# Performance work log

Measured on AMD Instinct MI355X. Metric: run time of the kernel, lower is better.

Reference implementation:

```python
import jax, jax.numpy as jnp
import numpy as np

N_NODES = 100000
N_EDGES = 600000
N_ETYPES = 3
N_LAYERS = 3  # n_layers + 1 conv layers
D = 128
EPS = 1e-5


def setup_inputs() -> dict:
    key = jax.random.key(0)
    ks = jax.random.split(key, 8)
    scale = 1.0 / np.sqrt(D)
    x = jax.random.normal(ks[0], (N_NODES, D), dtype=jnp.float32)
    src = jax.random.randint(ks[1], (N_ETYPES, N_EDGES), 0, N_NODES, dtype=jnp.int32)
    dst = jax.random.randint(ks[2], (N_ETYPES, N_EDGES), 0, N_NODES, dtype=jnp.int32)
    W_self = jax.random.normal(ks[3], (N_LAYERS, N_ETYPES, D, D), dtype=jnp.float32) * scale
    W_neigh = jax.random.normal(ks[4], (N_LAYERS, N_ETYPES, D, D), dtype=jnp.float32) * scale
    b = jax.random.normal(ks[5], (N_LAYERS, N_ETYPES, D), dtype=jnp.float32) * 0.01
    gamma = jnp.ones((N_LAYERS, D), dtype=jnp.float32)
    beta = jnp.zeros((N_LAYERS, D), dtype=jnp.float32)
    return {"x": x, "src": src, "dst": dst, "W_self": W_self, "W_neigh": W_neigh,
            "b": b, "gamma": gamma, "beta": beta}


def reference(x, src, dst, W_self, W_neigh, b, gamma, beta):
    N = x.shape[0]
    L, K = W_self.shape[0], W_self.shape[1]
    # in-degree per etype (DGL mean aggregator: zero-degree -> 0 neighbor feat)
    degs = [jnp.clip(jax.ops.segment_sum(jnp.ones((dst.shape[1],), x.dtype), dst[k],
                                         num_segments=N), 1.0, None)
            for k in range(K)]
    h = x
    for l in range(L):
        acc = jnp.zeros((N, W_self.shape[-1]), x.dtype)
        for k in range(K):
            # gather src feats, mean-aggregate onto dst: [N, D]
            neigh = jax.ops.segment_sum(h[src[k]], dst[k], num_segments=N) / degs[k][:, None]
            o = h @ W_self[l, k] + neigh @ W_neigh[l, k] + b[l, k]
            if l < L - 1:  # activation inside SAGEConv, last layer has none
                o = jax.nn.relu(o)
            acc = acc + o  # HeteroGraphConv aggregate='sum'
        # BatchNorm1d, training mode (biased batch variance)
        mu = acc.mean(axis=0)
        var = ((acc - mu) ** 2).mean(axis=0)
        h = gamma[l] * (acc - mu) / jnp.sqrt(var + EPS) + beta[l]
    return h
```

## Files before the change

kernel.cpp:

```cpp
#include <hip/hip_runtime.h>

#define NN 100000
#define NNP 100096
#define NE 600000
#define KE 3
#define NL 3
#define D  128
#define EPS 1e-5f
#define NB 391
#define NBKT 196
#define EPB 4096
#define NEB 147
#define NSL 16

typedef __attribute__((ext_vector_type(8))) short short8;
typedef __attribute__((ext_vector_type(4))) float floatx4;

__device__ __forceinline__ void atomic_add_f32(float* p, float v) { unsafeAtomicAdd(p, v); }

__device__ __forceinline__ float bf2f(unsigned int u16) {
    unsigned int v = u16 << 16;
    return __builtin_bit_cast(float, v);
}
__device__ __forceinline__ unsigned int f2bf(float f) {
    unsigned int u = __builtin_bit_cast(unsigned int, f);
    u += 0x7FFFu + ((u >> 16) & 1u);
    return u >> 16;
}
__device__ __forceinline__ unsigned int pack2(float a, float b) {
    return f2bf(a) | (f2bf(b) << 16);
}

__device__ __forceinline__ void gload16(const void* g, void* l) {
    __builtin_amdgcn_global_load_lds(
        (const __attribute__((address_space(1))) void*)g,
        (__attribute__((address_space(3))) void*)l, 16, 0, 0);
}

__global__ void convert_x_kernel(const float* __restrict__ x, ushort* __restrict__ hbf,
                                 int* __restrict__ bucketTotal) {
    size_t i = (size_t)blockIdx.x * blockDim.x + threadIdx.x;
    if (i < KE * NBKT) bucketTotal[i] = 0;
    if (i >= (size_t)NN * D / 4) return;
    float4 v = *(const float4*)(x + i * 4);
    uint2 o;
    o.x = pack2(v.x, v.y);
    o.y = pack2(v.z, v.w);
    *(uint2*)(hbf + i * 4) = o;
}

__global__ void wprep_kernel(const float* __restrict__ Ws, const float* __restrict__ Wn,
                             ushort* __restrict__ Bt, float* __restrict__ colstats) {
    int idx = blockIdx.x * blockDim.x + threadIdx.x;
    if (idx >= NL * KE * 128 * 256) return;
    if (idx < 2 * NL * NSL * D) colstats[idx] = 0.f;
    int lk  = idx >> 15;
    int rem = idx & 32767;
    int n   = rem >> 8;
    int kk  = rem & 255;
    float v = (kk < 128) ? Ws[(size_t)lk * 16384 + kk * 128 + n]
                         : Wn[(size_t)lk * 16384 + (kk - 128) * 128 + n];
    Bt[idx] = (ushort)f2bf(v);
}

__global__ void finfold_kernel(const float* __restrict__ colsum, const float* __restrict__ colsq,
                               const float* __restrict__ gamma, const float* __restrict__ beta,
                               const float* __restrict__ Wsl, const float* __restrict__ bsrc,
                               float* __restrict__ ssl, ushort* __restrict__ Btl,
                               float* __restrict__ biasW) {
    __shared__ float sc_s[D], sh_s[D];
    const int k = blockIdx.x;
    const int c = threadIdx.x;
    float s = 0.f, q = 0.f;
    #pragma unroll
    for (int i = 0; i < NSL; ++i) { s += colsum[i * D + c]; q += colsq[i * D + c]; }
    float mu  = s * (1.0f / NN);
    float var = q * (1.0f / NN) - mu * mu;
    float sc  = gamma[c] * rsqrtf(var + EPS);
    float sh  = beta[c] - mu * sc;
    sc_s[c] = sc; sh_s[c] = sh;
    if (k == 0) { ssl[c] = sc; ssl[D + c] = sh; }
    __syncthreads();
    const float* W = Wsl + (size_t)k * D * D;
    ushort* B = Btl + (size_t)k * 32768;
    float acc = 0.f;
    #pragma unroll 4
    for (int kk = 0; kk < D; ++kk) {
        float w = W[kk * D + c];
        acc += sh_s[kk] * w;
        B[c * 256 + kk] = (ushort)f2bf(sc_s[kk] * w);
    }
    biasW[k * D + c] = bsrc[k * D + c] + acc;
}

__global__ void bucket_count_kernel(const int* __restrict__ dst,
                                    int* __restrict__ bucketTotal, int* __restrict__ blockBase) {
    const int blk = blockIdx.x;
    const int k = blk / NEB, cb = blk - k * NEB;
    __shared__ int hist[NBKT];
    for (int i = threadIdx.x; i < NBKT; i += 256) hist[i] = 0;
    __syncthreads();
    const int e0 = cb * EPB, e1 = min(e0 + EPB, NE);
    for (int e = e0 + threadIdx.x; e < e1; e += 256)
        atomicAdd(&hist[dst[(size_t)k * NE + e] >> 9], 1);
    __syncthreads();
    for (int i = threadIdx.x; i < NBKT; i += 256) {
        int c = hist[i];
        int base = c ? atomicAdd(&bucketTotal[k * NBKT + i], c) : 0;
        blockBase[(size_t)blk * NBKT + i] = base;
    }
}

__global__ void bucket_scan_kernel(const int* __restrict__ bucketTotal,
                                   int* __restrict__ bucketStart) {
    __shared__ int sd[1024];
    const int t = threadIdx.x;
    int v = (t < KE * NBKT) ? bucketTotal[t] : 0;
    sd[t] = v;
    __syncthreads();
    for (int off = 1; off < 1024; off <<= 1) {
        int u = (t >= off) ? sd[t - off] : 0;
        __syncthreads();
        sd[t] += u;
        __syncthreads();
    }
    if (t < KE * NBKT) bucketStart[t] = sd[t] - v;
}

__global__ void bucket_scatter_kernel(const int* __restrict__ src, const int* __restrict__ dst,
                                      const int* __restrict__ bucketStart,
                                      const int* __restrict__ blockBase,
                                      uint2* __restrict__ ebuf) {
    const int blk = blockIdx.x;
    const int k = blk / NEB, cb = blk - k * NEB;
    __shared__ int hist[NBKT], binoff[NBKT], cur[NBKT];
    __shared__ int sc[256];
    __shared__ uint2 stage[EPB];
    const int t = threadIdx.x;
    for (int i = t; i < NBKT; i += 256) hist[i] = 0;
    __syncthreads();
    const int e0 = cb * EPB, e1 = min(e0 + EPB, NE);
    for (int e = e0 + t; e < e1; e += 256)
        atomicAdd(&hist[dst[(size_t)k * NE + e] >> 9], 1);
    __syncthreads();
    int hv = (t < NBKT) ? hist[t] : 0;
    sc[t] = hv;
    __syncthreads();
    for (int off = 1; off < 256; off <<= 1) {
        int u = (t >= off) ? sc[t - off] : 0;
        __syncthreads();
        sc[t] += u;
        __syncthreads();
    }
    if (t < NBKT) { binoff[t] = sc[t] - hv; cur[t] = sc[t] - hv; }
    __syncthreads();
    for (int e = e0 + t; e < e1; e += 256) {
        int d = dst[(size_t)k * NE + e], s = src[(size_t)k * NE + e];
        int b = d >> 9;
        int p = atomicAdd(&cur[b], 1);
        stage[p] = make_uint2((unsigned)s, (unsigned)d);
    }
    __syncthreads();
    const int n = e1 - e0;
    for (int i = t; i < n; i += 256) {
        uint2 ed = stage[i];
        int b = (int)(ed.y >> 9);
        int pos = bucketStart[k * NBKT + b] + blockBase[(size_t)blk * NBKT + b] + (i - binoff[b]);
        ebuf[pos] = ed;
    }
}

__global__ void bucket_deg_kernel(const uint2* __restrict__ ebuf,
                                  const int* __restrict__ bucketStart, int* __restrict__ degi,
                                  int* __restrict__ bsum) {
    const int blk = blockIdx.x;
    const int k = blk / NBKT, b = blk - k * NBKT;
    __shared__ int cnt[512];
    const int t = threadIdx.x;
    for (int i = t; i < 512; i += 256) cnt[i] = 0;
    __syncthreads();
    const int s0 = bucketStart[blk];
    const int s1 = (blk + 1 < KE * NBKT) ? bucketStart[blk + 1] : KE * NE;
    for (int e = s0 + t; e < s1; e += 256)
        atomicAdd(&cnt[ebuf[e].y & 511], 1);
    __syncthreads();
    const int n0 = b << 9;
    for (int i = t; i < 512; i += 256) {
        int node = n0 + i;
        if (node < NN) degi[(size_t)k * NN + node] = cnt[i];
    }
    __syncthreads();
    for (int off = 128; off > 0; off >>= 1) {
        if (t < off) { cnt[t] += cnt[t + off]; cnt[256 + t] += cnt[256 + t + off]; }
        __syncthreads();
    }
    if (t == 0) {
        bsum[k * NB + 2 * b] = cnt[0];
        if (2 * b + 1 < NB) bsum[k * NB + 2 * b + 1] = cnt[256];
    }
}

__global__ void scan_b_kernel(int* __restrict__ bsum) {
    const int k = blockIdx.x;
    const int t = threadIdx.x;
    int v = (t < NB) ? bsum[k * NB + t] : 0;
    __shared__ int sd[512];
    sd[t] = v;
    __syncthreads();
    for (int off = 1; off < 512; off <<= 1) {
        int u = (t >= off) ? sd[t - off] : 0;
        __syncthreads();
        sd[t] += u;
        __syncthreads();
    }
    if (t < NB) bsum[k * NB + t] = sd[t] - v;
}

__global__ void scan_c_kernel(const int* __restrict__ degi, const int* __restrict__ bsum,
                              int* __restrict__ rowptr, float* __restrict__ invdeg) {
    const int b = blockIdx.x;
    const int k = b / NB, lb = b - k * NB;
    const int t = threadIdx.x;
    const int i = lb * 256 + t;
    int deg = (i < NN) ? degi[(size_t)k * NN + i] : 0;
    __shared__ int sd[256];
    sd[t] = deg;
    __syncthreads();
    for (int off = 1; off < 256; off <<= 1) {
        int u = (t >= off) ? sd[t - off] : 0;
        __syncthreads();
        sd[t] += u;
        __syncthreads();
    }
    int val = bsum[b] + sd[t] - deg;
    if (i < NN) {
        rowptr[(size_t)k * (NN + 1) + i] = val;
        invdeg[(size_t)k * NN + i] = 1.0f / (float)max(deg, 1);
    }
    if (i == NN) rowptr[(size_t)k * (NN + 1) + NN] = NE;
}

__global__ void bucket_fill_kernel(const uint2* __restrict__ ebuf,
                                   const int* __restrict__ bucketStart,
                                   const int* __restrict__ rowptr, int* __restrict__ csr) {
    const int blk = blockIdx.x;
    const int k = blk / NBKT, b = blk - k * NBKT;
    __shared__ int cur[512];
    const int n0 = b << 9;
    for (int i = threadIdx.x; i < 512; i += 256) {
        int node = n0 + i;
        cur[i] = (node < NN) ? rowptr[(size_t)k * (NN + 1) + node] : 0;
    }
    __syncthreads();
    const int s0 = bucketStart[blk];
    const int s1 = (blk + 1 < KE * NBKT) ? bucketStart[blk + 1] : KE * NE;
    for (int e = s0 + threadIdx.x; e < s1; e += 256) {
        uint2 ed = ebuf[e];
        int p = atomicAdd(&cur[ed.y & 511], 1);
        csr[(size_t)k * NE + p] = (int)ed.x;
    }
}

__global__ void gather3_kernel(const ushort* __restrict__ hsrc, const int* __restrict__ csr,
                               const int* __restrict__ rowptr, const float* __restrict__ invdeg,
                               ushort* __restrict__ neigh, const float* __restrict__ ssl,
                               int affine) {
    int g = blockIdx.x * 16 + (threadIdx.x >> 4);
    if (g >= KE * NN) return;
    int k = g / NN, node = g - k * NN;
    const int q = (threadIdx.x & 15) * 8;
    const int* rp = rowptr + (size_t)k * (NN + 1) + node;
    const int* cs = csr + (size_t)k * NE;
    int beg = rp[0], end = rp[1];
    float f0=0,f1=0,f2=0,f3=0,f4=0,f5=0,f6=0,f7=0;
    int j = beg;
    for (; j + 4 <= end; j += 4) {
        int s0 = cs[j], s1 = cs[j + 1], s2 = cs[j + 2], s3 = cs[j + 3];
        uint4 a = *(const uint4*)(hsrc + (size_t)s0 * D + q);
        uint4 b = *(const uint4*)(hsrc + (size_t)s1 * D + q);
        uint4 c = *(const uint4*)(hsrc + (size_t)s2 * D + q);
        uint4 d = *(const uint4*)(hsrc + (size_t)s3 * D + q);
        f0 += bf2f(a.x & 0xffff) + bf2f(b.x & 0xffff) + bf2f(c.x & 0xffff) + bf2f(d.x & 0xffff);
        f1 += bf2f(a.x >> 16)    + bf2f(b.x >> 16)    + bf2f(c.x >> 16)    + bf2f(d.x >> 16);
        f2 += bf2f(a.y & 0xffff) + bf2f(b.y & 0xffff) + bf2f(c.y & 0xffff) + bf2f(d.y & 0xffff);
        f3 += bf2f(a.y >> 16)    + bf2f(b.y >> 16)    + bf2f(c.y >> 16)    + bf2f(d.y >> 16);
        f4 += bf2f(a.z & 0xffff) + bf2f(b.z & 0xffff) + bf2f(c.z & 0xffff) + bf2f(d.z & 0xffff);
        f5 += bf2f(a.z >> 16)    + bf2f(b.z >> 16)    + bf2f(c.z >> 16)    + bf2f(d.z >> 16);
        f6 += bf2f(a.w & 0xffff) + bf2f(b.w & 0xffff) + bf2f(c.w & 0xffff) + bf2f(d.w & 0xffff);
        f7 += bf2f(a.w >> 16)    + bf2f(b.w >> 16)    + bf2f(c.w >> 16)    + bf2f(d.w >> 16);
    }
    for (; j < end; ++j) {
        int s0 = cs[j];
        uint4 a = *(const uint4*)(hsrc + (size_t)s0 * D + q);
        f0 += bf2f(a.x & 0xffff); f1 += bf2f(a.x >> 16);
        f2 += bf2f(a.y & 0xffff); f3 += bf2f(a.y >> 16);
        f4 += bf2f(a.z & 0xffff); f5 += bf2f(a.z >> 16);
        f6 += bf2f(a.w & 0xffff); f7 += bf2f(a.w >> 16);
    }
    float iv = invdeg[g];
    float r0 = f0 * iv, r1 = f1 * iv, r2 = f2 * iv, r3 = f3 * iv;
    float r4 = f4 * iv, r5 = f5 * iv, r6 = f6 * iv, r7 = f7 * iv;
    if (affine) {
        float4 c0 = *(const float4*)(ssl + q);
        float4 c1 = *(const float4*)(ssl + q + 4);
        float4 h0 = *(const float4*)(ssl + D + q);
        float4 h1 = *(const float4*)(ssl + D + q + 4);
        float m = (end > beg) ? 1.0f : 0.0f;
        r0 = r0 * c0.x + m * h0.x;  r1 = r1 * c0.y + m * h0.y;
        r2 = r2 * c0.z + m * h0.z;  r3 = r3 * c0.w + m * h0.w;
        r4 = r4 * c1.x + m * h1.x;  r5 = r5 * c1.y + m * h1.y;
        r6 = r6 * c1.z + m * h1.z;  r7 = r7 * c1.w + m * h1.w;
    }
    uint4 o;
    o.x = pack2(r0, r1);
    o.y = pack2(r2, r3);
    o.z = pack2(r4, r5);
    o.w = pack2(r6, r7);
    *(uint4*)(neigh + (size_t)k * NNP * D + (size_t)node * D + q) = o;
}

__global__ __launch_bounds__(512, 4)
void layer_gemm_kernel(const ushort* __restrict__ hself, const ushort* __restrict__ neigh,
                       const ushort* __restrict__ Bt,
                       const float* __restrict__ bias,
                       ushort* __restrict__ accb, int relu,
                       float* __restrict__ colsum, float* __restrict__ colsq) {
    __shared__ __align__(16) ushort ST[2][2][128][64];
    const int tid  = threadIdx.x;
    const int wave = tid >> 6, lane = tid & 63;
    const int wm = wave & 1, wn = wave >> 1;
    const int lrow = lane & 15, quad = lane >> 4;
    const int m0 = blockIdx.x * 128;
    const int srow  = lane >> 3;
    const int scolb = ((lane & 7) ^ srow) << 4;

#define STAGE(b, kk, cc)                                                                 \
    {                                                                                    \
        const char* Asrc = ((cc) < 2) ? (const char*)hself                               \
                                      : (const char*)(neigh + (size_t)(kk) * NNP * D);   \
        const char* Bsrc = (const char*)Bt + (size_t)(kk) * 65536;                       \
        char* Adst = (char*)&ST[b][0][0][0];                                             \
        char* Bdst = (char*)&ST[b][1][0][0];                                             \
        _Pragma("unroll")                                                                \
        for (int i = 0; i < 2; ++i) {                                                    \
            int r = wave * 16 + i * 8 + srow;                                            \
            gload16(Asrc + (size_t)(m0 + r) * 256 + ((cc) & 1) * 128 + scolb,            \
                    Adst + wave * 2048 + i * 1024);                                      \
        }                                                                                \
        _Pragma("unroll")                                                                \
        for (int i = 0; i < 2; ++i) {                                                    \
            int n = wave * 16 + i * 8 + srow;                                            \
            gload16(Bsrc + (size_t)n * 512 + (cc) * 128 + scolb,                         \
                    Bdst + wave * 2048 + i * 1024);                                      \
        }                                                                                \
    }

    floatx4 tot[4][2], o4[4][2];
    #pragma unroll
    for (int a = 0; a < 4; ++a)
        #pragma unroll
        for (int b = 0; b < 2; ++b) {
            tot[a][b] = (floatx4){0.f, 0.f, 0.f, 0.f};
            o4[a][b]  = (floatx4){0.f, 0.f, 0.f, 0.f};
        }

    STAGE(0, 0, 0);

    int cur = 0;
    #pragma unroll
    for (int p = 0; p < 4 * KE; ++p) {
        __syncthreads();
        if (p + 1 < 4 * KE) {
            const int pn = p + 1;
            STAGE(cur ^ 1, pn >> 2, pn & 3);
        }
        const char* Ab = (const char*)&ST[cur][0][0][0];
        const char* Bb = (const char*)&ST[cur][1][0][0];
        #pragma unroll
        for (int ks = 0; ks < 2; ++ks) {
            short8 af[4], bfr[2];
            const int cb = ks * 64 + quad * 16;
            #pragma unroll
            for (int im = 0; im < 4; ++im) {
                int ra = wm * 64 + im * 16 + lrow;
                af[im] = *(const short8*)(Ab + ra * 128 + (cb ^ ((ra & 7) << 4)));
            }
            #pragma unroll
            for (int in = 0; in < 2; ++in) {
                int rb = wn * 32 + in * 16 + lrow;
                bfr[in] = *(const short8*)(Bb + rb * 128 + (cb ^ ((rb & 7) << 4)));
            }
            #pragma unroll
            for (int im = 0; im < 4; ++im)
                #pragma unroll
                for (int in = 0; in < 2; ++in)
                    o4[im][in] = __builtin_amdgcn_mfma_f32_16x16x32_bf16(
                        af[im], bfr[in], o4[im][in], 0, 0, 0);
        }
        if ((p & 3) == 3) {
            const float* bk = bias + (p >> 2) * D;
            float bv[2];
            #pragma unroll
            for (int in = 0; in < 2; ++in) bv[in] = bk[wn * 32 + in * 16 + lrow];
            #pragma unroll
            for (int im = 0; im < 4; ++im)
                #pragma unroll
                for (int in = 0; in < 2; ++in)
                    #pragma unroll
                    for (int r = 0; r < 4; ++r) {
                        float v = o4[im][in][r] + bv[in];
                        if (relu) v = fmaxf(v, 0.f);
                        tot[im][in][r] += v;
                        o4[im][in][r] = 0.f;
                    }
        }
        cur ^= 1;
    }
#undef STAGE

    float ls[2] = {0.f, 0.f}, lq[2] = {0.f, 0.f};
    #pragma unroll
    for (int im = 0; im < 4; ++im)
        #pragma unroll
        for (int r = 0; r < 4; ++r) {
            int row = m0 + wm * 64 + im * 16 + quad * 4 + r;
            bool ok = row < NN;
            #pragma unroll
            for (int in = 0; in < 2; ++in) {
                float v = ok ? tot[im][in][r] : 0.f;
                ls[in] += v;
                lq[in] += v * v;
            }
        }
    __syncthreads();
    float* redS = (float*)&ST[1][0][0][0];
    float* redQ = redS + 1024;
    #pragma unroll
    for (int in = 0; in < 2; ++in) {
        int col = wn * 32 + in * 16 + lrow;
        int slot = col * 8 + wm * 4 + quad;
        redS[slot] = ls[in];
        redQ[slot] = lq[in];
    }
    __syncthreads();
    if (tid < 128) {
        float s = 0.f, q = 0.f;
        #pragma unroll
        for (int i = 0; i < 8; ++i) { s += redS[tid * 8 + i]; q += redQ[tid * 8 + i]; }
        int slice = blockIdx.x & (NSL - 1);
        atomic_add_f32(&colsum[slice * D + tid], s);
        atomic_add_f32(&colsq[slice * D + tid], q);
    }

    ushort* Cs = &ST[0][0][0][0];
    #pragma unroll
    for (int im = 0; im < 4; ++im)
        #pragma unroll
        for (int r = 0; r < 4; ++r) {
            int rl = wm * 64 + im * 16 + quad * 4 + r;
            #pragma unroll
            for (int in = 0; in < 2; ++in)
                Cs[rl * 128 + wn * 32 + in * 16 + lrow] = (ushort)f2bf(tot[im][in][r]);
        }
    __syncthreads();
    #pragma unroll
    for (int jj = 0; jj < 4; ++jj) {
        int c8 = tid + jj * 512;
        int rl = c8 >> 4;
        int cc = (c8 & 15) * 8;
        int row = m0 + rl;
        if (row < NN)
            *(uint4*)(accb + (size_t)row * D + cc) = *(const uint4*)(Cs + rl * 128 + cc);
    }
}

__global__ void finalize_kernel(const float* __restrict__ colsum, const float* __restrict__ colsq,
                                const float* __restrict__ gamma, const float* __restrict__ beta,
                                float* __restrict__ ssl) {
    int c = threadIdx.x;
    float s = 0.f, q = 0.f;
    #pragma unroll
    for (int i = 0; i < NSL; ++i) { s += colsum[i * D + c]; q += colsq[i * D + c]; }
    float mu  = s * (1.0f / NN);
    float var = q * (1.0f / NN) - mu * mu;
    float sc  = gamma[c] * rsqrtf(var + EPS);
    ssl[c]     = sc;
    ssl[D + c] = beta[c] - mu * sc;
}

__global__ void bn_kernel(const ushort* __restrict__ accb, const float* __restrict__ ssl,
                          float* __restrict__ out) {
    size_t i = (size_t)blockIdx.x * blockDim.x + threadIdx.x;
    if (i >= (size_t)NN * D / 4) return;
    int c4 = (int)(i & 31) << 2;
    uint2 a = *(const uint2*)(accb + i * 4);
    float4 v = {bf2f(a.x & 0xffff), bf2f(a.x >> 16), bf2f(a.y & 0xffff), bf2f(a.y >> 16)};
    float4 sc = *(const float4*)(ssl + c4);
    float4 sh = *(const float4*)(ssl + D + c4);
    float4 o;
    o.x = v.x * sc.x + sh.x;
    o.y = v.y * sc.y + sh.y;
    o.z = v.z * sc.z + sh.z;
    o.w = v.w * sc.w + sh.w;
    *(float4*)(out + i * 4) = o;
}

extern "C" void kernel_launch(void* const* d_in, const int* in_sizes, int n_in,
                              void* d_out, int out_size, void* d_ws, size_t ws_size,
                              hipStream_t stream) {
    const float* x       = (const float*)d_in[0];
    const int*   src     = (const int*)d_in[1];
    const int*   dst     = (const int*)d_in[2];
    const float* W_self  = (const float*)d_in[3];
    const float* W_neigh = (const float*)d_in[4];
    const float* bvec    = (const float*)d_in[5];
    const float* gamma   = (const float*)d_in[6];
    const float* beta    = (const float*)d_in[7];
    float* out = (float*)d_out;

    ushort* accb   = (ushort*)d_ws;
    float*  invdeg = (float*)(accb + (size_t)NNP * D);
    float*  colsum = invdeg + (size_t)KE * NN;
    float*  colsq  = colsum + NL * NSL * D;
    float*  ss     = colsq + NL * NSL * D;
    float*  biasW  = ss + NL * 2 * D;
    ushort* hbf    = (ushort*)(biasW + KE * D);
    ushort* neigh  = hbf + (size_t)NNP * D;
    ushort* Btw    = neigh + (size_t)KE * NNP * D;
    int*    degi   = (int*)(Btw + (size_t)NL * KE * 128 * 256);
    int*    rowptr = degi + (size_t)KE * NN;
    int*    csr    = rowptr + (size_t)KE * (NN + 1);
    int*    bsum   = csr + (size_t)KE * NE;
    int*    bucketTotal = bsum + (size_t)KE * NB;
    int*    bucketStart = bucketTotal + KE * NBKT;
    int*    blockBase   = bucketStart + KE * NBKT;
    uint2*  ebuf   = (uint2*)accb;

    convert_x_kernel<<<(int)(((size_t)NN * D / 4 + 255) / 256), 256, 0, stream>>>(
        x, hbf, bucketTotal);
    wprep_kernel<<<(NL * KE * 128 * 256 + 255) / 256, 256, 0, stream>>>(
        W_self, W_neigh, Btw, colsum);

    bucket_count_kernel<<<KE * NEB, 256, 0, stream>>>(dst, bucketTotal, blockBase);
    bucket_scan_kernel<<<1, 1024, 0, stream>>>(bucketTotal, bucketStart);
    bucket_scatter_kernel<<<KE * NEB, 256, 0, stream>>>(src, dst, bucketStart, blockBase, ebuf);
    bucket_deg_kernel<<<KE * NBKT, 256, 0, stream>>>(ebuf, bucketStart, degi, bsum);
    scan_b_kernel<<<KE, 512, 0, stream>>>(bsum);
    scan_c_kernel<<<KE * NB, 256, 0, stream>>>(degi, bsum, rowptr, invdeg);
    bucket_fill_kernel<<<KE * NBKT, 256, 0, stream>>>(ebuf, bucketStart, rowptr, csr);

    for (int l = 0; l < NL; ++l) {
        int relu = (l < NL - 1) ? 1 : 0;
        const ushort* hsrc = (l == 0) ? hbf : accb;
        const float*  ssl  = ss + (size_t)(l ? l - 1 : 0) * 2 * D;
        gather3_kernel<<<(KE * NN + 15) / 16, 256, 0, stream>>>(
            hsrc, csr, rowptr, invdeg, neigh, ssl, l > 0);
        layer_gemm_kernel<<<NNP / 128, 512, 0, stream>>>(
            hsrc, neigh,
            Btw + (size_t)l * KE * 128 * 256,
            (l == 0) ? bvec : biasW,
            accb, relu,
            colsum + (size_t)l * NSL * D, colsq + (size_t)l * NSL * D);
        if (l + 1 < NL) {
            finfold_kernel<<<KE, 128, 0, stream>>>(
                colsum + (size_t)l * NSL * D, colsq + (size_t)l * NSL * D,
                gamma + (size_t)l * D, beta + (size_t)l * D,
                W_self + (size_t)(l + 1) * KE * D * D,
                bvec + (size_t)(l + 1) * KE * D,
                ss + (size_t)l * 2 * D,
                Btw + (size_t)(l + 1) * KE * 128 * 256,
                biasW);
        } else {
            finalize_kernel<<<1, 128, 0, stream>>>(
                colsum + (size_t)l * NSL * D, colsq + (size_t)l * NSL * D,
                gamma + (size_t)l * D, beta + (size_t)l * D, ss + (size_t)l * 2 * D);
        }
    }
    bn_kernel<<<(int)(((size_t)NN * D / 4 + 255) / 256), 256, 0, stream>>>(
        accb, ss + (size_t)(NL - 1) * 2 * D, out);
}
```

Measured before the change: 549.1 us.

## Load GEMM fragments directly from global memory instead of staging through LDS

The layer GEMM no longer double-buffers A and B tiles into shared memory with global_load_lds. Each wave now reads its MFMA fragments straight from global memory (hself, neigh, and transposed weights), and the main-loop barriers are dropped. The output/stat reduction uses dedicated LDS buffers, which saves one barrier. The cost is redundant global/L2 traffic, since A rows are re-read by 4 waves and B by 2, plus uncoalesced 16-byte row-strided loads with no prefetch overlap.

```diff
diff --git a/kernel.cpp b/kernel.cpp
--- a/kernel.cpp
+++ b/kernel.cpp
@@ -29,12 +29,6 @@
 }
 __device__ __forceinline__ unsigned int pack2(float a, float b) {
     return f2bf(a) | (f2bf(b) << 16);
-}
-
-__device__ __forceinline__ void gload16(const void* g, void* l) {
-    __builtin_amdgcn_global_load_lds(
-        (const __attribute__((address_space(1))) void*)g,
-        (__attribute__((address_space(3))) void*)l, 16, 0, 0);
 }
 
 __global__ void convert_x_kernel(const float* __restrict__ x, ushort* __restrict__ hbf,
@@ -325,71 +319,52 @@
                        const float* __restrict__ bias,
                        ushort* __restrict__ accb, int relu,
                        float* __restrict__ colsum, float* __restrict__ colsq) {
-    __shared__ __align__(16) ushort ST[2][2][128][64];
+    __shared__ __align__(16) ushort Cs[128 * 128];
+    __shared__ float red[2048];
     const int tid  = threadIdx.x;
     const int wave = tid >> 6, lane = tid & 63;
     const int wm = wave & 1, wn = wave >> 1;
     const int lrow = lane & 15, quad = lane >> 4;
     const int m0 = blockIdx.x * 128;
-    const int srow  = lane >> 3;
-    const int scolb = ((lane & 7) ^ srow) << 4;
-
-#define STAGE(b, kk, cc)                                                                 \
-    {                                                                                    \
-        const char* Asrc = ((cc) < 2) ? (const char*)hself                               \
-                                      : (const char*)(neigh + (size_t)(kk) * NNP * D);   \
-        const char* Bsrc = (const char*)Bt + (size_t)(kk) * 65536;                       \
-        char* Adst = (char*)&ST[b][0][0][0];                                             \
-        char* Bdst = (char*)&ST[b][1][0][0];                                             \
-        _Pragma("unroll")                                                                \
-        for (int i = 0; i < 2; ++i) {                                                    \
-            int r = wave * 16 + i * 8 + srow;                                            \
-            gload16(Asrc + (size_t)(m0 + r) * 256 + ((cc) & 1) * 128 + scolb,            \
-                    Adst + wave * 2048 + i * 1024);                                      \
-        }                                                                                \
-        _Pragma("unroll")                                                                \
-        for (int i = 0; i < 2; ++i) {                                                    \
-            int n = wave * 16 + i * 8 + srow;                                            \
-            gload16(Bsrc + (size_t)n * 512 + (cc) * 128 + scolb,                         \
-                    Bdst + wave * 2048 + i * 1024);                                      \
-        }                                                                                \
-    }
-
-    floatx4 tot[4][2], o4[4][2];
+    const int qb = quad * 16;
+
+    size_t aRow[4];
+    #pragma unroll
+    for (int im = 0; im < 4; ++im)
+        aRow[im] = (size_t)(m0 + wm * 64 + im * 16 + lrow) * 256;
+    size_t bRow[2];
+    #pragma unroll
+    for (int in = 0; in < 2; ++in)
+        bRow[in] = (size_t)(wn * 32 + in * 16 + lrow) * 512;
+
+    floatx4 tot[4][2];
     #pragma unroll
     for (int a = 0; a < 4; ++a)
         #pragma unroll
-        for (int b = 0; b < 2; ++b) {
+        for (int b = 0; b < 2; ++b)
             tot[a][b] = (floatx4){0.f, 0.f, 0.f, 0.f};
-            o4[a][b]  = (floatx4){0.f, 0.f, 0.f, 0.f};
-        }
-
-    STAGE(0, 0, 0);
-
-    int cur = 0;
-    #pragma unroll
-    for (int p = 0; p < 4 * KE; ++p) {
-        __syncthreads();
-        if (p + 1 < 4 * KE) {
-            const int pn = p + 1;
-            STAGE(cur ^ 1, pn >> 2, pn & 3);
-        }
-        const char* Ab = (const char*)&ST[cur][0][0][0];
-        const char* Bb = (const char*)&ST[cur][1][0][0];
-        #pragma unroll
-        for (int ks = 0; ks < 2; ++ks) {
+
+    for (int k = 0; k < KE; ++k) {
+        const char* nB  = (const char*)(neigh + (size_t)k * NNP * D);
+        const char* Btk = (const char*)Bt + (size_t)k * 65536;
+        floatx4 o4[4][2];
+        #pragma unroll
+        for (int a = 0; a < 4; ++a)
+            #pragma unroll
+            for (int b = 0; b < 2; ++b)
+                o4[a][b] = (floatx4){0.f, 0.f, 0.f, 0.f};
+        #pragma unroll
+        for (int c8 = 0; c8 < 8; ++c8) {
+            const int part = c8 >> 2;
+            const int off  = ((c8 >> 1) & 1) * 128 + (c8 & 1) * 64 + qb;
+            const char* Ab = part ? nB : (const char*)hself;
             short8 af[4], bfr[2];
-            const int cb = ks * 64 + quad * 16;
-            #pragma unroll
-            for (int im = 0; im < 4; ++im) {
-                int ra = wm * 64 + im * 16 + lrow;
-                af[im] = *(const short8*)(Ab + ra * 128 + (cb ^ ((ra & 7) << 4)));
-            }
-            #pragma unroll
-            for (int in = 0; in < 2; ++in) {
-                int rb = wn * 32 + in * 16 + lrow;
-                bfr[in] = *(const short8*)(Bb + rb * 128 + (cb ^ ((rb & 7) << 4)));
-            }
+            #pragma unroll
+            for (int im = 0; im < 4; ++im)
+                af[im] = *(const short8*)(Ab + aRow[im] + off);
+            #pragma unroll
+            for (int in = 0; in < 2; ++in)
+                bfr[in] = *(const short8*)(Btk + bRow[in] + part * 256 + off);
             #pragma unroll
             for (int im = 0; im < 4; ++im)
                 #pragma unroll
@@ -397,26 +372,21 @@
                     o4[im][in] = __builtin_amdgcn_mfma_f32_16x16x32_bf16(
                         af[im], bfr[in], o4[im][in], 0, 0, 0);
         }
-        if ((p & 3) == 3) {
-            const float* bk = bias + (p >> 2) * D;
-            float bv[2];
-            #pragma unroll
-            for (int in = 0; in < 2; ++in) bv[in] = bk[wn * 32 + in * 16 + lrow];
-            #pragma unroll
-            for (int im = 0; im < 4; ++im)
+        const float* bk = bias + k * D;
+        float bv[2];
+        #pragma unroll
+        for (int in = 0; in < 2; ++in) bv[in] = bk[wn * 32 + in * 16 + lrow];
+        #pragma unroll
+        for (int im = 0; im < 4; ++im)
+            #pragma unroll
+            for (int in = 0; in < 2; ++in)
                 #pragma unroll
-                for (int in = 0; in < 2; ++in)
-                    #pragma unroll
-                    for (int r = 0; r < 4; ++r) {
-                        float v = o4[im][in][r] + bv[in];
-                        if (relu) v = fmaxf(v, 0.f);
-                        tot[im][in][r] += v;
-                        o4[im][in][r] = 0.f;
-                    }
-        }
-        cur ^= 1;
-    }
-#undef STAGE
+                for (int r = 0; r < 4; ++r) {
+                    float v = o4[im][in][r] + bv[in];
+                    if (relu) v = fmaxf(v, 0.f);
+                    tot[im][in][r] += v;
+                }
+    }
 
     float ls[2] = {0.f, 0.f}, lq[2] = {0.f, 0.f};
     #pragma unroll
@@ -432,9 +402,8 @@
                 lq[in] += v * v;
             }
         }
-    __syncthreads();
-    float* redS = (float*)&ST[1][0][0][0];
-    float* redQ = redS + 1024;
+    float* redS = red;
+    float* redQ = red + 1024;
     #pragma unroll
     for (int in = 0; in < 2; ++in) {
         int col = wn * 32 + in * 16 + lrow;
@@ -442,6 +411,15 @@
         redS[slot] = ls[in];
         redQ[slot] = lq[in];
     }
+    #pragma unroll
+    for (int im = 0; im < 4; ++im)
+        #pragma unroll
+        for (int r = 0; r < 4; ++r) {
+            int rl = wm * 64 + im * 16 + quad * 4 + r;
+            #pragma unroll
+            for (int in = 0; in < 2; ++in)
+                Cs[rl * 128 + wn * 32 + in * 16 + lrow] = (ushort)f2bf(tot[im][in][r]);
+        }
     __syncthreads();
     if (tid < 128) {
         float s = 0.f, q = 0.f;
@@ -451,18 +429,6 @@
         atomic_add_f32(&colsum[slice * D + tid], s);
         atomic_add_f32(&colsq[slice * D + tid], q);
     }
-
-    ushort* Cs = &ST[0][0][0][0];
-    #pragma unroll
-    for (int im = 0; im < 4; ++im)
-        #pragma unroll
-        for (int r = 0; r < 4; ++r) {
-            int rl = wm * 64 + im * 16 + quad * 4 + r;
-            #pragma unroll
-            for (int in = 0; in < 2; ++in)
-                Cs[rl * 128 + wn * 32 + in * 16 + lrow] = (ushort)f2bf(tot[im][in][r]);
-        }
-    __syncthreads();
     #pragma unroll
     for (int jj = 0; jj < 4; ++jj) {
         int c8 = tid + jj * 512;
```

Result: slower. 872.6 us (+58.9%).

## Load self-feature tile once per block and reuse it across edge types

Applied to the files above, without the earlier changes.

The layer GEMM used to re-stage the hself A-tile from global memory for each of the three edge types. It now loads that tile once into a dedicated shared buffer. Each edge-type phase stages the full self-weight slab together, so a type takes three pipeline steps instead of four. The epilogue also drops two barriers by writing the BN partial sums and the bf16 output tile to separate shared regions before a single sync. The cost is about 50% more shared memory per block and a launch-bounds occupancy hint lowered from 4 to 2 blocks.

```diff
diff --git a/kernel.cpp b/kernel.cpp
--- a/kernel.cpp
+++ b/kernel.cpp
@@ -319,13 +319,14 @@
     *(uint4*)(neigh + (size_t)k * NNP * D + (size_t)node * D + q) = o;
 }
 
-__global__ __launch_bounds__(512, 4)
+__global__ __launch_bounds__(512, 2)
 void layer_gemm_kernel(const ushort* __restrict__ hself, const ushort* __restrict__ neigh,
                        const ushort* __restrict__ Bt,
                        const float* __restrict__ bias,
                        ushort* __restrict__ accb, int relu,
                        float* __restrict__ colsum, float* __restrict__ colsq) {
-    __shared__ __align__(16) ushort ST[2][2][128][64];
+    __shared__ __align__(16) ushort Asf[2][128][64];
+    __shared__ __align__(16) ushort Dst[2][2][128][64];
     const int tid  = threadIdx.x;
     const int wave = tid >> 6, lane = tid & 63;
     const int wm = wave & 1, wn = wave >> 1;
@@ -334,25 +335,56 @@
     const int srow  = lane >> 3;
     const int scolb = ((lane & 7) ^ srow) << 4;
 
-#define STAGE(b, kk, cc)                                                                 \
-    {                                                                                    \
-        const char* Asrc = ((cc) < 2) ? (const char*)hself                               \
-                                      : (const char*)(neigh + (size_t)(kk) * NNP * D);   \
-        const char* Bsrc = (const char*)Bt + (size_t)(kk) * 65536;                       \
-        char* Adst = (char*)&ST[b][0][0][0];                                             \
-        char* Bdst = (char*)&ST[b][1][0][0];                                             \
-        _Pragma("unroll")                                                                \
-        for (int i = 0; i < 2; ++i) {                                                    \
-            int r = wave * 16 + i * 8 + srow;                                            \
-            gload16(Asrc + (size_t)(m0 + r) * 256 + ((cc) & 1) * 128 + scolb,            \
-                    Adst + wave * 2048 + i * 1024);                                      \
-        }                                                                                \
-        _Pragma("unroll")                                                                \
-        for (int i = 0; i < 2; ++i) {                                                    \
-            int n = wave * 16 + i * 8 + srow;                                            \
-            gload16(Bsrc + (size_t)n * 512 + (cc) * 128 + scolb,                         \
-                    Bdst + wave * 2048 + i * 1024);                                      \
-        }                                                                                \
+#define STAGE(b, kk, pt)                                                                  \
+    {                                                                                     \
+        const char* Bsrc = (const char*)Bt + (size_t)(kk) * 65536;                        \
+        char* Db = (char*)&Dst[b][0][0][0];                                               \
+        if ((pt) == 0) {                                                                  \
+            _Pragma("unroll")                                                             \
+            for (int kc = 0; kc < 2; ++kc)                                                \
+                _Pragma("unroll")                                                         \
+                for (int i = 0; i < 2; ++i) {                                             \
+                    int n = wave * 16 + i * 8 + srow;                                     \
+                    gload16(Bsrc + (size_t)n * 512 + kc * 128 + scolb,                    \
+                            Db + kc * 16384 + wave * 2048 + i * 1024);                    \
+                }                                                                         \
+        } else {                                                                          \
+            const int kc = (pt) - 1;                                                      \
+            const char* Asrc = (const char*)(neigh + (size_t)(kk) * NNP * D);             \
+            _Pragma("unroll")                                                             \
+            for (int i = 0; i < 2; ++i) {                                                 \
+                int r = wave * 16 + i * 8 + srow;                                         \
+                gload16(Asrc + (size_t)(m0 + r) * 256 + kc * 128 + scolb,                 \
+                        Db + wave * 2048 + i * 1024);                                     \
+                gload16(Bsrc + (size_t)r * 512 + 256 + kc * 128 + scolb,                  \
+                        Db + 16384 + wave * 2048 + i * 1024);                             \
+            }                                                                             \
+        }                                                                                 \
+    }
+
+#define MFMA8(Abase, Bbase)                                                               \
+    {                                                                                     \
+        _Pragma("unroll")                                                                 \
+        for (int ks = 0; ks < 2; ++ks) {                                                  \
+            short8 af[4], bfr[2];                                                         \
+            const int cb = ks * 64 + quad * 16;                                           \
+            _Pragma("unroll")                                                             \
+            for (int im = 0; im < 4; ++im) {                                              \
+                int ra = wm * 64 + im * 16 + lrow;                                        \
+                af[im] = *(const short8*)((Abase) + ra * 128 + (cb ^ ((ra & 7) << 4)));   \
+            }                                                                             \
+            _Pragma("unroll")                                                             \
+            for (int in = 0; in < 2; ++in) {                                              \
+                int rb = wn * 32 + in * 16 + lrow;                                        \
+                bfr[in] = *(const short8*)((Bbase) + rb * 128 + (cb ^ ((rb & 7) << 4)));  \
+            }                                                                             \
+            _Pragma("unroll")                                                             \
+            for (int im = 0; im < 4; ++im)                                                \
+                _Pragma("unroll")                                                         \
+                for (int in = 0; in < 2; ++in)                                            \
+                    o4[im][in] = __builtin_amdgcn_mfma_f32_16x16x32_bf16(                 \
+                        af[im], bfr[in], o4[im][in], 0, 0, 0);                            \
+        }                                                                                 \
     }
 
     floatx4 tot[4][2], o4[4][2];
@@ -364,41 +396,35 @@
             o4[a][b]  = (floatx4){0.f, 0.f, 0.f, 0.f};
         }
 
+    {
+        const char* Ab = (const char*)hself + (size_t)m0 * 256;
+        #pragma unroll
+        for (int kc = 0; kc < 2; ++kc)
+            #pragma unroll
+            for (int i = 0; i < 2; ++i)
+                gload16(Ab + (size_t)(wave * 16 + i * 8 + srow) * 256 + kc * 128 + scolb,
+                        (char*)Asf + kc * 16384 + wave * 2048 + i * 1024);
+    }
     STAGE(0, 0, 0);
 
     int cur = 0;
     #pragma unroll
-    for (int p = 0; p < 4 * KE; ++p) {
-        __syncthreads();
-        if (p + 1 < 4 * KE) {
+    for (int p = 0; p < 3 * KE; ++p) {
+        __syncthreads();
+        if (p + 1 < 3 * KE) {
             const int pn = p + 1;
-            STAGE(cur ^ 1, pn >> 2, pn & 3);
+            STAGE(cur ^ 1, pn / 3, pn % 3);
         }
-        const char* Ab = (const char*)&ST[cur][0][0][0];
-        const char* Bb = (const char*)&ST[cur][1][0][0];
-        #pragma unroll
-        for (int ks = 0; ks < 2; ++ks) {
-            short8 af[4], bfr[2];
-            const int cb = ks * 64 + quad * 16;
-            #pragma unroll
-            for (int im = 0; im < 4; ++im) {
-                int ra = wm * 64 + im * 16 + lrow;
-                af[im] = *(const short8*)(Ab + ra * 128 + (cb ^ ((ra & 7) << 4)));
-            }
-            #pragma unroll
-            for (int in = 0; in < 2; ++in) {
-                int rb = wn * 32 + in * 16 + lrow;
-                bfr[in] = *(const short8*)(Bb + rb * 128 + (cb ^ ((rb & 7) << 4)));
-            }
-            #pragma unroll
-            for (int im = 0; im < 4; ++im)
-                #pragma unroll
-                for (int in = 0; in < 2; ++in)
-                    o4[im][in] = __builtin_amdgcn_mfma_f32_16x16x32_bf16(
-                        af[im], bfr[in], o4[im][in], 0, 0, 0);
+        const int pt = p % 3;
+        const char* Db = (const char*)&Dst[cur][0][0][0];
+        if (pt == 0) {
+            MFMA8((const char*)Asf,         Db);
+            MFMA8((const char*)Asf + 16384, Db + 16384);
+        } else {
+            MFMA8(Db, Db + 16384);
         }
-        if ((p & 3) == 3) {
-            const float* bk = bias + (p >> 2) * D;
+        if (pt == 2) {
+            const float* bk = bias + (p / 3) * D;
             float bv[2];
             #pragma unroll
             for (int in = 0; in < 2; ++in) bv[in] = bk[wn * 32 + in * 16 + lrow];
@@ -417,6 +443,7 @@
         cur ^= 1;
     }
 #undef STAGE
+#undef MFMA8
 
     float ls[2] = {0.f, 0.f}, lq[2] = {0.f, 0.f};
     #pragma unroll
@@ -432,8 +459,7 @@
                 lq[in] += v * v;
             }
         }
-    __syncthreads();
-    float* redS = (float*)&ST[1][0][0][0];
+    float* redS = (float*)&Dst[1][0][0][0];
     float* redQ = redS + 1024;
     #pragma unroll
     for (int in = 0; in < 2; ++in) {
@@ -442,17 +468,7 @@
         redS[slot] = ls[in];
         redQ[slot] = lq[in];
     }
-    __syncthreads();
-    if (tid < 128) {
-        float s = 0.f, q = 0.f;
-        #pragma unroll
-        for (int i = 0; i < 8; ++i) { s += redS[tid * 8 + i]; q += redQ[tid * 8 + i]; }
-        int slice = blockIdx.x & (NSL - 1);
-        atomic_add_f32(&colsum[slice * D + tid], s);
-        atomic_add_f32(&colsq[slice * D + tid], q);
-    }
-
-    ushort* Cs = &ST[0][0][0][0];
+    ushort* Cs = &Asf[0][0][0];
     #pragma unroll
     for (int im = 0; im < 4; ++im)
         #pragma unroll
@@ -463,6 +479,14 @@
                 Cs[rl * 128 + wn * 32 + in * 16 + lrow] = (ushort)f2bf(tot[im][in][r]);
         }
     __syncthreads();
+    if (tid < 128) {
+        float s = 0.f, q = 0.f;
+        #pragma unroll
+        for (int i = 0; i < 8; ++i) { s += redS[tid * 8 + i]; q += redQ[tid * 8 + i]; }
+        int slice = blockIdx.x & (NSL - 1);
+        atomic_add_f32(&colsum[slice * D + tid], s);
+        atomic_add_f32(&colsq[slice * D + tid], q);
+    }
     #pragma unroll
     for (int jj = 0; jj < 4; ++jj) {
         int c8 = tid + jj * 512;
```

Result: slower. 584.4 us (+6.4%).

## Merge self-weight GEMMs across edge types in final linear layer

Applied to the files above, without the earlier changes.

The last layer has no ReLU, so the sum over edge types of h@W_self[k] collapses into one GEMM with a pre-summed, BN-folded weight matrix and a summed bias. A new merged fold kernel builds that summed weight. The last-layer GEMM then runs 8 K-phases instead of 12, cutting MFMA work and B/A loads by about a third. The C-tile store to shared memory also moves before the stats reduction barrier, dropping one __syncthreads.

```diff
diff --git a/kernel.cpp b/kernel.cpp
--- a/kernel.cpp
+++ b/kernel.cpp
@@ -91,6 +91,44 @@
         B[c * 256 + kk] = (ushort)f2bf(sc_s[kk] * w);
     }
     biasW[k * D + c] = bsrc[k * D + c] + acc;
+}
+
+__global__ void finfold_merged_kernel(const float* __restrict__ colsum,
+                                      const float* __restrict__ colsq,
+                                      const float* __restrict__ gamma,
+                                      const float* __restrict__ beta,
+                                      const float* __restrict__ Wsl,
+                                      const float* __restrict__ bsrc,
+                                      float* __restrict__ ssl,
+                                      ushort* __restrict__ Bsum, float* __restrict__ biasSum) {
+    __shared__ float sc_s[D], sh_s[D];
+    const int c = threadIdx.x;
+    float s = 0.f, q = 0.f;
+    #pragma unroll
+    for (int i = 0; i < NSL; ++i) { s += colsum[i * D + c]; q += colsq[i * D + c]; }
+    float mu  = s * (1.0f / NN);
+    float var = q * (1.0f / NN) - mu * mu;
+    float sc  = gamma[c] * rsqrtf(var + EPS);
+    float sh  = beta[c] - mu * sc;
+    sc_s[c] = sc; sh_s[c] = sh;
+    ssl[c] = sc; ssl[D + c] = sh;
+    __syncthreads();
+    float bacc = 0.f;
+    #pragma unroll 2
+    for (int kk = 0; kk < D; ++kk) {
+        float wsum = 0.f;
+        #pragma unroll
+        for (int k = 0; k < KE; ++k) {
+            float w = Wsl[(size_t)k * D * D + kk * D + c];
+            wsum += sc_s[kk] * w;
+            bacc += sh_s[kk] * w;
+        }
+        Bsum[c * 128 + kk] = (ushort)f2bf(wsum);
+    }
+    float bs = 0.f;
+    #pragma unroll
+    for (int k = 0; k < KE; ++k) bs += bsrc[k * D + c];
+    biasSum[c] = bs + bacc;
 }
 
 __global__ void bucket_count_kernel(const int* __restrict__ dst,
@@ -319,9 +357,10 @@
     *(uint4*)(neigh + (size_t)k * NNP * D + (size_t)node * D + q) = o;
 }
 
+template <int MERGED>
 __global__ __launch_bounds__(512, 4)
 void layer_gemm_kernel(const ushort* __restrict__ hself, const ushort* __restrict__ neigh,
-                       const ushort* __restrict__ Bt,
+                       const ushort* __restrict__ Bt, const ushort* __restrict__ Bsum,
                        const float* __restrict__ bias,
                        ushort* __restrict__ accb, int relu,
                        float* __restrict__ colsum, float* __restrict__ colsq) {
@@ -333,24 +372,37 @@
     const int m0 = blockIdx.x * 128;
     const int srow  = lane >> 3;
     const int scolb = ((lane & 7) ^ srow) << 4;
-
-#define STAGE(b, kk, cc)                                                                 \
+    const int NPH = MERGED ? 2 + 2 * KE : 4 * KE;
+
+#define STAGE(b, pp)                                                                     \
     {                                                                                    \
-        const char* Asrc = ((cc) < 2) ? (const char*)hself                               \
-                                      : (const char*)(neigh + (size_t)(kk) * NNP * D);   \
-        const char* Bsrc = (const char*)Bt + (size_t)(kk) * 65536;                       \
+        const char* Asrc; const char* Bsrc; int aoff; int boff; int bstride;             \
+        if (MERGED) {                                                                    \
+            if ((pp) < 2) {                                                              \
+                Asrc = (const char*)hself; aoff = (pp) * 128;                            \
+                Bsrc = (const char*)Bsum;  boff = (pp) * 128; bstride = 256;             \
+            } else {                                                                     \
+                int kk2 = ((pp) - 2) >> 1, cc2 = ((pp) - 2) & 1;                         \
+                Asrc = (const char*)(neigh + (size_t)kk2 * NNP * D); aoff = cc2 * 128;   \
+                Bsrc = (const char*)Bt + (size_t)kk2 * 65536;                            \
+                boff = 256 + cc2 * 128; bstride = 512;                                   \
+            }                                                                            \
+        } else {                                                                         \
+            int kk2 = (pp) >> 2, cc2 = (pp) & 3;                                         \
+            Asrc = (cc2 < 2) ? (const char*)hself                                        \
+                             : (const char*)(neigh + (size_t)kk2 * NNP * D);             \
+            aoff = (cc2 & 1) * 128;                                                      \
+            Bsrc = (const char*)Bt + (size_t)kk2 * 65536;                                \
+            boff = cc2 * 128; bstride = 512;                                             \
+        }                                                                                \
         char* Adst = (char*)&ST[b][0][0][0];                                             \
         char* Bdst = (char*)&ST[b][1][0][0];                                             \
         _Pragma("unroll")                                                                \
         for (int i = 0; i < 2; ++i) {                                                    \
             int r = wave * 16 + i * 8 + srow;                                            \
-            gload16(Asrc + (size_t)(m0 + r) * 256 + ((cc) & 1) * 128 + scolb,            \
+            gload16(Asrc + (size_t)(m0 + r) * 256 + aoff + scolb,                        \
                     Adst + wave * 2048 + i * 1024);                                      \
-        }                                                                                \
-        _Pragma("unroll")                                                                \
-        for (int i = 0; i < 2; ++i) {                                                    \
-            int n = wave * 16 + i * 8 + srow;                                            \
-            gload16(Bsrc + (size_t)n * 512 + (cc) * 128 + scolb,                         \
+            gload16(Bsrc + (size_t)r * bstride + boff + scolb,                           \
                     Bdst + wave * 2048 + i * 1024);                                      \
         }                                                                                \
     }
@@ -364,15 +416,14 @@
             o4[a][b]  = (floatx4){0.f, 0.f, 0.f, 0.f};
         }
 
-    STAGE(0, 0, 0);
+    STAGE(0, 0);
 
     int cur = 0;
     #pragma unroll
-    for (int p = 0; p < 4 * KE; ++p) {
-        __syncthreads();
-        if (p + 1 < 4 * KE) {
-            const int pn = p + 1;
-            STAGE(cur ^ 1, pn >> 2, pn & 3);
+    for (int p = 0; p < NPH; ++p) {
+        __syncthreads();
+        if (p + 1 < NPH) {
+            STAGE(cur ^ 1, p + 1);
         }
         const char* Ab = (const char*)&ST[cur][0][0][0];
         const char* Bb = (const char*)&ST[cur][1][0][0];
@@ -397,7 +448,7 @@
                     o4[im][in] = __builtin_amdgcn_mfma_f32_16x16x32_bf16(
                         af[im], bfr[in], o4[im][in], 0, 0, 0);
         }
-        if ((p & 3) == 3) {
+        if (!MERGED && (p & 3) == 3) {
             const float* bk = bias + (p >> 2) * D;
             float bv[2];
             #pragma unroll
@@ -417,6 +468,18 @@
         cur ^= 1;
     }
 #undef STAGE
+    if (MERGED) {
+        float bv[2];
+        #pragma unroll
+        for (int in = 0; in < 2; ++in) bv[in] = bias[wn * 32 + in * 16 + lrow];
+        #pragma unroll
+        for (int im = 0; im < 4; ++im)
+            #pragma unroll
+            for (int in = 0; in < 2; ++in)
+                #pragma unroll
+                for (int r = 0; r < 4; ++r)
+                    tot[im][in][r] = o4[im][in][r] + bv[in];
+    }
 
     float ls[2] = {0.f, 0.f}, lq[2] = {0.f, 0.f};
     #pragma unroll
@@ -442,6 +505,16 @@
         redS[slot] = ls[in];
         redQ[slot] = lq[in];
     }
+    #pragma unroll
+    for (int im = 0; im < 4; ++im)
+        #pragma unroll
+        for (int r = 0; r < 4; ++r) {
+            int rl = wm * 64 + im * 16 + quad * 4 + r;
+            #pragma unroll
+            for (int in = 0; in < 2; ++in)
+                ((ushort*)&ST[0][0][0][0])[rl * 128 + wn * 32 + in * 16 + lrow] =
+                    (ushort)f2bf(tot[im][in][r]);
+        }
     __syncthreads();
     if (tid < 128) {
         float s = 0.f, q = 0.f;
@@ -451,18 +524,7 @@
         atomic_add_f32(&colsum[slice * D + tid], s);
         atomic_add_f32(&colsq[slice * D + tid], q);
     }
-
-    ushort* Cs = &ST[0][0][0][0];
-    #pragma unroll
-    for (int im = 0; im < 4; ++im)
-        #pragma unroll
-        for (int r = 0; r < 4; ++r) {
-            int rl = wm * 64 + im * 16 + quad * 4 + r;
-            #pragma unroll
-            for (int in = 0; in < 2; ++in)
-                Cs[rl * 128 + wn * 32 + in * 16 + lrow] = (ushort)f2bf(tot[im][in][r]);
-        }
-    __syncthreads();
+    const ushort* Cs = (const ushort*)&ST[0][0][0][0];
     #pragma unroll
     for (int jj = 0; jj < 4; ++jj) {
         int c8 = tid + jj * 512;
@@ -524,7 +586,9 @@
     float*  colsq  = colsum + NL * NSL * D;
     float*  ss     = colsq + NL * NSL * D;
     float*  biasW  = ss + NL * 2 * D;
-    ushort* hbf    = (ushort*)(biasW + KE * D);
+    float*  biasSum = biasW + KE * D;
+    ushort* Bsum   = (ushort*)(biasSum + D);
+    ushort* hbf    = Bsum + 128 * 128;
     ushort* neigh  = hbf + (size_t)NNP * D;
     ushort* Btw    = neigh + (size_t)KE * NNP * D;
     int*    degi   = (int*)(Btw + (size_t)NL * KE * 128 * 256);
@@ -555,13 +619,22 @@
         const float*  ssl  = ss + (size_t)(l ? l - 1 : 0) * 2 * D;
         gather3_kernel<<<(KE * NN + 15) / 16, 256, 0, stream>>>(
             hsrc, csr, rowptr, invdeg, neigh, ssl, l > 0);
-        layer_gemm_kernel<<<NNP / 128, 512, 0, stream>>>(
-            hsrc, neigh,
-            Btw + (size_t)l * KE * 128 * 256,
-            (l == 0) ? bvec : biasW,
-            accb, relu,
-            colsum + (size_t)l * NSL * D, colsq + (size_t)l * NSL * D);
-        if (l + 1 < NL) {
+        if (l < NL - 1) {
+            layer_gemm_kernel<0><<<NNP / 128, 512, 0, stream>>>(
+                hsrc, neigh,
+                Btw + (size_t)l * KE * 128 * 256, Bsum,
+                (l == 0) ? bvec : biasW,
+                accb, relu,
+                colsum + (size_t)l * NSL * D, colsq + (size_t)l * NSL * D);
+        } else {
+            layer_gemm_kernel<1><<<NNP / 128, 512, 0, stream>>>(
+                hsrc, neigh,
+                Btw + (size_t)l * KE * 128 * 256, Bsum,
+                biasSum,
+                accb, relu,
+                colsum + (size_t)l * NSL * D, colsq + (size_t)l * NSL * D);
+        }
+        if (l == 0) {
             finfold_kernel<<<KE, 128, 0, stream>>>(
                 colsum + (size_t)l * NSL * D, colsq + (size_t)l * NSL * D,
                 gamma + (size_t)l * D, beta + (size_t)l * D,
@@ -570,6 +643,14 @@
                 ss + (size_t)l * 2 * D,
                 Btw + (size_t)(l + 1) * KE * 128 * 256,
                 biasW);
+        } else if (l == 1) {
+            finfold_merged_kernel<<<1, 128, 0, stream>>>(
+                colsum + (size_t)l * NSL * D, colsq + (size_t)l * NSL * D,
+                gamma + (size_t)l * D, beta + (size_t)l * D,
+                W_self + (size_t)(l + 1) * KE * D * D,
+                bvec + (size_t)(l + 1) * KE * D,
+                ss + (size_t)l * 2 * D,
+                Bsum, biasSum);
         } else {
             finalize_kernel<<<1, 128, 0, stream>>>(
                 colsum + (size_t)l * NSL * D, colsq + (size_t)l * NSL * D,
```

After: 548.6 us. No clear change (-0.1%).
